# Kernel tuning notes

Measured on AMD Instinct MI355X. Metric: run time of the kernel, lower is better.

Reference implementation:

```python
import jax, jax.numpy as jnp
import numpy as np


def setup_inputs() -> dict:
    key = jax.random.key(0)
    k1, k2 = jax.random.split(key)
    B, C, H, W = 8, 19, 512, 1024
    inputs = jax.random.normal(k1, (B, C, H, W), dtype=jnp.float32)
    targets = jax.random.randint(k2, (B, H, W), 0, C, dtype=jnp.int32)
    return {"inputs": inputs, "targets": targets}


def reference(inputs, targets):
    # inputs: [B, C, H, W] logits; targets: [B, H, W] int class ids
    C = inputs.shape[1]
    logp = jax.nn.log_softmax(inputs, axis=1)            # [B, C, H, W]
    t = targets.reshape(-1)                              # [N]
    # per-class inverse-frequency weights via single-pass histogram
    counts = jnp.zeros((C,), dtype=jnp.float32).at[t].add(1.0)
    inv_freq = jnp.where(counts > 0, 1.0 / jnp.maximum(counts, 1.0), 1.0)  # [C]
    weight = inv_freq[t]                                 # [N]
    # gather log-prob of the target class per pixel
    logp_flat = jnp.transpose(logp, (0, 2, 3, 1)).reshape(-1, C)  # [N, C]
    nll = -jnp.take_along_axis(logp_flat, t[:, None], axis=1)[:, 0]  # [N]
    return jnp.sum(weight * nll) / jnp.sum(weight)
```

## Files before the change

### kernel.cpp

```cpp
#include <hip/hip_runtime.h>

#define NUM_C 19
#define HW_SHIFT 19
#define HW (1 << HW_SHIFT)
#define NPIX (8 * HW)
#define NGROUPS (NPIX / 4)
#define BLOCK 256
#define GRID 2048
#define NTH (GRID * BLOCK)
#define SLOTS 40

__global__ __launch_bounds__(BLOCK) void ifl_main(const float* __restrict__ x,
                                                  const int* __restrict__ tgt,
                                                  float* __restrict__ part) {
    float acc[NUM_C], cnt[NUM_C];
#pragma unroll
    for (int c = 0; c < NUM_C; ++c) { acc[c] = 0.0f; cnt[c] = 0.0f; }

    const int tid = blockIdx.x * BLOCK + threadIdx.x;

#pragma unroll
    for (int it = 0; it < NGROUPS / NTH; ++it) {
        const int g = tid + it * NTH;
        const int p = g << 2;
        const int b = p >> HW_SHIFT;
        const int r = p & (HW - 1);
        const float* base = x + (((size_t)b * NUM_C) << HW_SHIFT) + r;

        const int4 t4 = *reinterpret_cast<const int4*>(tgt + p);

        float s0 = 0.f, s1 = 0.f, s2 = 0.f, s3 = 0.f;
        float x0 = 0.f, x1 = 0.f, x2 = 0.f, x3 = 0.f;
#pragma unroll
        for (int c = 0; c < NUM_C; ++c) {
            const float4 v = *reinterpret_cast<const float4*>(base + ((size_t)c << HW_SHIFT));
            s0 += __expf(v.x); s1 += __expf(v.y); s2 += __expf(v.z); s3 += __expf(v.w);
            x0 = (t4.x == c) ? v.x : x0;
            x1 = (t4.y == c) ? v.y : x1;
            x2 = (t4.z == c) ? v.z : x2;
            x3 = (t4.w == c) ? v.w : x3;
        }
        const float n0 = __logf(s0) - x0;
        const float n1 = __logf(s1) - x1;
        const float n2 = __logf(s2) - x2;
        const float n3 = __logf(s3) - x3;
#pragma unroll
        for (int c = 0; c < NUM_C; ++c) {
            acc[c] += ((t4.x == c) ? n0 : 0.f) + ((t4.y == c) ? n1 : 0.f)
                    + ((t4.z == c) ? n2 : 0.f) + ((t4.w == c) ? n3 : 0.f);
            cnt[c] += ((t4.x == c) ? 1.f : 0.f) + ((t4.y == c) ? 1.f : 0.f)
                    + ((t4.z == c) ? 1.f : 0.f) + ((t4.w == c) ? 1.f : 0.f);
        }
    }

    __shared__ float red[SLOTS];
    if (threadIdx.x < SLOTS) red[threadIdx.x] = 0.0f;
    __syncthreads();

#pragma unroll
    for (int c = 0; c < NUM_C; ++c) {
        float a = acc[c];
        float n = cnt[c];
#pragma unroll
        for (int off = 32; off > 0; off >>= 1) {
            a += __shfl_down(a, off, 64);
            n += __shfl_down(n, off, 64);
        }
        if ((threadIdx.x & 63) == 0) {
            atomicAdd(&red[c], a);
            atomicAdd(&red[NUM_C + c], n);
        }
    }
    __syncthreads();
    if (threadIdx.x < SLOTS) part[blockIdx.x * SLOTS + threadIdx.x] = red[threadIdx.x];
}

__global__ __launch_bounds__(BLOCK) void ifl_final(const float* __restrict__ part,
                                                   float* __restrict__ out) {
    __shared__ float red[SLOTS];
    if (threadIdx.x < SLOTS) red[threadIdx.x] = 0.0f;
    __syncthreads();

    float acc[SLOTS];
#pragma unroll
    for (int s = 0; s < SLOTS; ++s) acc[s] = 0.0f;

    for (int k = threadIdx.x; k < GRID; k += BLOCK) {
        const float4* p4 = reinterpret_cast<const float4*>(part + (size_t)k * SLOTS);
#pragma unroll
        for (int q = 0; q < SLOTS / 4; ++q) {
            const float4 v = p4[q];
            acc[4 * q + 0] += v.x;
            acc[4 * q + 1] += v.y;
            acc[4 * q + 2] += v.z;
            acc[4 * q + 3] += v.w;
        }
    }

#pragma unroll
    for (int s = 0; s < SLOTS; ++s) {
        float v = acc[s];
#pragma unroll
        for (int off = 32; off > 0; off >>= 1) v += __shfl_down(v, off, 64);
        if ((threadIdx.x & 63) == 0) atomicAdd(&red[s], v);
    }
    __syncthreads();

    if (threadIdx.x == 0) {
        float num = 0.f, den = 0.f;
#pragma unroll
        for (int c = 0; c < NUM_C; ++c) {
            const float cn = red[NUM_C + c];
            const float inv = (cn > 0.f) ? (1.f / fmaxf(cn, 1.f)) : 1.f;
            num += inv * red[c];
            den += inv * cn;
        }
        out[0] = num / den;
    }
}

extern "C" void kernel_launch(void* const* d_in, const int* in_sizes, int n_in,
                              void* d_out, int out_size, void* d_ws, size_t ws_size,
                              hipStream_t stream) {
    const float* x = (const float*)d_in[0];
    const int* tgt = (const int*)d_in[1];
    float* ws = (float*)d_ws;
    float* out = (float*)d_out;

    ifl_main<<<GRID, BLOCK, 0, stream>>>(x, tgt, ws);
    ifl_main<<<GRID, BLOCK, 0, stream>>>(x, tgt, ws);
    ifl_final<<<1, BLOCK, 0, stream>>>(ws, out);
}
```

Before: 524.1 us.

## Remove duplicate main launch, batch logit loads, use max-subtracted stable log-softmax

Drops the redundant second launch of the main kernel, which recomputed the same partials into the same workspace. The main loop now issues all 19 float4 loads up front, then computes per-pixel max-subtracted exp sums, so the log-softmax is numerically stable. The extra max pass adds VALU work and the 76 loaded values raise register pressure, but only one full read of the input remains.

```diff
diff --git a/kernel.cpp b/kernel.cpp
--- a/kernel.cpp
+++ b/kernel.cpp
@@ -19,37 +19,44 @@
 
     const int tid = blockIdx.x * BLOCK + threadIdx.x;
 
+    union F4 { float4 q; float f[4]; };
+    union I4 { int4 q; int i[4]; };
+
 #pragma unroll
     for (int it = 0; it < NGROUPS / NTH; ++it) {
         const int g = tid + it * NTH;
         const int p = g << 2;
         const int b = p >> HW_SHIFT;
         const int r = p & (HW - 1);
-        const float* base = x + (((size_t)b * NUM_C) << HW_SHIFT) + r;
+        const float4* base4 =
+            reinterpret_cast<const float4*>(x + (((size_t)b * NUM_C) << HW_SHIFT) + r);
 
-        const int4 t4 = *reinterpret_cast<const int4*>(tgt + p);
+        F4 v[NUM_C];
+#pragma unroll
+        for (int c = 0; c < NUM_C; ++c) v[c].q = base4[(size_t)c << (HW_SHIFT - 2)];
 
-        float s0 = 0.f, s1 = 0.f, s2 = 0.f, s3 = 0.f;
-        float x0 = 0.f, x1 = 0.f, x2 = 0.f, x3 = 0.f;
+        I4 tt;
+        tt.q = *reinterpret_cast<const int4*>(tgt + p);
+
 #pragma unroll
-        for (int c = 0; c < NUM_C; ++c) {
-            const float4 v = *reinterpret_cast<const float4*>(base + ((size_t)c << HW_SHIFT));
-            s0 += __expf(v.x); s1 += __expf(v.y); s2 += __expf(v.z); s3 += __expf(v.w);
-            x0 = (t4.x == c) ? v.x : x0;
-            x1 = (t4.y == c) ? v.y : x1;
-            x2 = (t4.z == c) ? v.z : x2;
-            x3 = (t4.w == c) ? v.w : x3;
-        }
-        const float n0 = __logf(s0) - x0;
-        const float n1 = __logf(s1) - x1;
-        const float n2 = __logf(s2) - x2;
-        const float n3 = __logf(s3) - x3;
+        for (int k = 0; k < 4; ++k) {
+            const int tg = tt.i[k];
+            float m = v[0].f[k];
 #pragma unroll
-        for (int c = 0; c < NUM_C; ++c) {
-            acc[c] += ((t4.x == c) ? n0 : 0.f) + ((t4.y == c) ? n1 : 0.f)
-                    + ((t4.z == c) ? n2 : 0.f) + ((t4.w == c) ? n3 : 0.f);
-            cnt[c] += ((t4.x == c) ? 1.f : 0.f) + ((t4.y == c) ? 1.f : 0.f)
-                    + ((t4.z == c) ? 1.f : 0.f) + ((t4.w == c) ? 1.f : 0.f);
+            for (int c = 1; c < NUM_C; ++c) m = fmaxf(m, v[c].f[k]);
+            float s = 0.0f;
+#pragma unroll
+            for (int c = 0; c < NUM_C; ++c) s += __expf(v[c].f[k] - m);
+            float xt = v[0].f[k];
+#pragma unroll
+            for (int c = 1; c < NUM_C; ++c) xt = (tg == c) ? v[c].f[k] : xt;
+            const float nll = m + __logf(s) - xt;
+#pragma unroll
+            for (int c = 0; c < NUM_C; ++c) {
+                const bool h = (tg == c);
+                acc[c] += h ? nll : 0.0f;
+                cnt[c] += h ? 1.0f : 0.0f;
+            }
         }
     }
 
@@ -128,6 +135,5 @@
     float* out = (float*)d_out;
 
     ifl_main<<<GRID, BLOCK, 0, stream>>>(x, tgt, ws);
-    ifl_main<<<GRID, BLOCK, 0, stream>>>(x, tgt, ws);
     ifl_final<<<1, BLOCK, 0, stream>>>(ws, out);
 }
```

Measured after the change: 450.6 us, median of 2. -14.0%, faster.
